# Kernel tuning notes

Hardware: AMD Instinct MI355X
Metric: run time of the kernel (lower is better)

Reference implementation:

```python
import jax, jax.numpy as jnp
import numpy as np
from jax import lax

B, P, C = 2, 512, 5                 # images, proposals/img, classes (incl. background)
IN_FEAT, REP = 12544, 1024          # 256*7*7 pooled features; TwoMLPHead width
H_IMG = W_IMG = 800.0
SCORE_THRESH, NMS_THRESH, DET_PER_IMG = 0.05, 0.5, 100
MIN_SIZE = 0.01
WX, WY, WW, WH = 10.0, 10.0, 5.0, 5.0
BBOX_CLIP = float(np.log(1000.0 / 16.0))
NEG = -1e9


def _make_boxes(key, n):
    k1, k2, k3, k4 = jax.random.split(key, 4)
    cx = jax.random.uniform(k1, (n,)) * W_IMG
    cy = jax.random.uniform(k2, (n,)) * H_IMG
    bw = jax.random.uniform(k3, (n,)) * 180.0 + 20.0
    bh = jax.random.uniform(k4, (n,)) * 180.0 + 20.0
    x1 = jnp.clip(cx - bw / 2, 0.0, W_IMG)
    y1 = jnp.clip(cy - bh / 2, 0.0, H_IMG)
    x2 = jnp.clip(cx + bw / 2, 0.0, W_IMG)
    y2 = jnp.clip(cy + bh / 2, 0.0, H_IMG)
    return jnp.stack([x1, y1, x2, y2], -1).astype(jnp.float32)


def setup_inputs() -> dict:
    ks = jax.random.split(jax.random.key(0), 12)
    box_features = jax.random.normal(ks[0], (B * P, IN_FEAT), jnp.float32)
    proposals = jnp.stack([_make_boxes(ks[1 + i], P) for i in range(B)])
    def w(k, shp):
        return (jax.random.normal(k, shp, jnp.float32) / np.sqrt(shp[0])).astype(jnp.float32)
    return {
        'box_features': box_features,
        'proposals': proposals,
        'W1': w(ks[3], (IN_FEAT, REP)), 'b1': jnp.zeros((REP,), jnp.float32),
        'W2': w(ks[4], (REP, REP)),     'b2': jnp.zeros((REP,), jnp.float32),
        'Wc': w(ks[5], (REP, C)),       'bc': jnp.zeros((C,), jnp.float32),
        'Wb': w(ks[6], (REP, 4 * C)),   'bb': jnp.zeros((4 * C,), jnp.float32),
    }


def box_iou(a, b):
    area_a = (a[:, 2] - a[:, 0]) * (a[:, 3] - a[:, 1])
    area_b = (b[:, 2] - b[:, 0]) * (b[:, 3] - b[:, 1])
    lt = jnp.maximum(a[:, None, :2], b[None, :, :2])
    rb = jnp.minimum(a[:, None, 2:], b[None, :, 2:])
    wh = jnp.clip(rb - lt, 0.0)
    inter = wh[..., 0] * wh[..., 1]
    return inter / (area_a[:, None] + area_b[None, :] - inter + 1e-9)


def decode(reg, props):
    # reg: [N, C, 4] raw deltas; props: [N, 4] xyxy  (torchvision BoxCoder.decode)
    w = props[:, 2] - props[:, 0]
    h = props[:, 3] - props[:, 1]
    cx = props[:, 0] + 0.5 * w
    cy = props[:, 1] + 0.5 * h
    dx, dy = reg[..., 0] / WX, reg[..., 1] / WY
    dw = jnp.minimum(reg[..., 2] / WW, BBOX_CLIP)
    dh = jnp.minimum(reg[..., 3] / WH, BBOX_CLIP)
    pcx = dx * w[:, None] + cx[:, None]
    pcy = dy * h[:, None] + cy[:, None]
    pw = jnp.exp(dw) * w[:, None]
    ph = jnp.exp(dh) * h[:, None]
    return jnp.stack([pcx - 0.5 * pw, pcy - 0.5 * ph, pcx + 0.5 * pw, pcy + 0.5 * ph], -1)


def postprocess_one(boxes, scores, labels):
    # boxes [M,4] (already clipped), scores [M], labels [M] int; fixed-size output.
    M = boxes.shape[0]
    ws = boxes[:, 2] - boxes[:, 0]
    hs = boxes[:, 3] - boxes[:, 1]
    valid = (scores > SCORE_THRESH) & (ws >= MIN_SIZE) & (hs >= MIN_SIZE)
    order = jnp.argsort(-scores)
    b, s, l, v = boxes[order], scores[order], labels[order], valid[order]
    # batched (per-class) NMS via class-offset trick
    off = l.astype(b.dtype)[:, None] * (max(H_IMG, W_IMG) + 1.0)
    iou = box_iou(b + off, b + off)
    idxs = jnp.arange(M)

    def body(i, keep):
        sup = (iou[i] > NMS_THRESH) & keep[i] & (idxs > i)
        return keep & ~sup

    keep = lax.fori_loop(0, M, body, v)
    sc = jnp.where(keep, s, NEG)
    top_s, top_i = lax.top_k(sc, DET_PER_IMG)
    ok = top_s > NEG / 2
    tb = jnp.where(ok[:, None], b[top_i], 0.0)
    tl = jnp.where(ok, l[top_i], 0)
    ts = jnp.where(ok, top_s, 0.0)
    return tb, ts, tl


def reference(box_features, proposals, W1, b1, W2, b2, Wc, bc, Wb, bb):
    # box_head: TwoMLPHead
    h = jax.nn.relu(box_features @ W1 + b1)
    h = jax.nn.relu(h @ W2 + b2)
    # box_predictor
    class_logits = h @ Wc + bc                       # [N, C]
    box_regression = (h @ Wb + bb).reshape(-1, C, 4)  # [N, C, 4]
    props = proposals.reshape(-1, 4)
    pred = decode(box_regression, props)             # [N, C, 4]
    # clip to image
    pred = jnp.stack([
        jnp.clip(pred[..., 0], 0.0, W_IMG), jnp.clip(pred[..., 1], 0.0, H_IMG),
        jnp.clip(pred[..., 2], 0.0, W_IMG), jnp.clip(pred[..., 3], 0.0, H_IMG)], -1)
    scores = jax.nn.softmax(class_logits, -1)        # [N, C]
    # drop background class, flatten proposal-major (matches torch reshape(-1,4))
    pb = pred[:, 1:, :].reshape(B, P * (C - 1), 4)
    sc = scores[:, 1:].reshape(B, P * (C - 1))
    labels = jnp.tile(jnp.arange(1, C, dtype=jnp.int32), P)  # [M]
    boxes_o, scores_o, labels_o = jax.vmap(postprocess_one, in_axes=(0, 0, None))(pb, sc, labels)
    return boxes_o, scores_o, labels_o
```

## Files before the change

### kernel.cpp

```cpp
#include <hip/hip_runtime.h>
#include <math.h>

#define NROWS 1024
#define K1    12544
#define REP   1024
#define NDET  2048
#define DETS  100
#define BBOX_CLIP_F 4.135166556742356f

typedef __attribute__((ext_vector_type(8))) short bf16x8;
typedef __attribute__((ext_vector_type(4))) float f32x4;

__device__ __forceinline__ unsigned short rne_bf16(float x) {
  unsigned u = __float_as_uint(x);
  u += 0x7fffu + ((u >> 16) & 1u);
  return (unsigned short)(u >> 16);
}
__device__ __forceinline__ float bf16f(unsigned short h) {
  return __uint_as_float(((unsigned)h) << 16);
}
__device__ __forceinline__ int swz(int r, int s) {
  return s ^ (r & 3) ^ ((r >> 2) & 3);
}
__device__ __forceinline__ void gload16(const void* g, void* lds) {
  __builtin_amdgcn_global_load_lds(
      (const __attribute__((address_space(1))) unsigned int*)g,
      (__attribute__((address_space(3))) unsigned int*)lds, 16, 0, 0);
}

__global__ __launch_bounds__(256) void pack_b(
    const float* __restrict__ W, unsigned short* __restrict__ Oh,
    unsigned short* __restrict__ Ol, int nKB) {
  __shared__ unsigned short th[32 * 36], tl[32 * 36];
  const int kb = blockIdx.x, n0 = blockIdx.y * 32;
  const int t = threadIdx.x;
  const int r = t >> 3, c4 = (t & 7) << 2;
  float4 v = *(const float4*)&W[(size_t)(kb * 32 + r) * REP + n0 + c4];
  float fv[4] = {v.x, v.y, v.z, v.w};
#pragma unroll
  for (int j = 0; j < 4; ++j) {
    unsigned short h = rne_bf16(fv[j]);
    th[(c4 + j) * 36 + r] = h;
    tl[(c4 + j) * 36 + r] = rne_bf16(fv[j] - bf16f(h));
  }
  __syncthreads();
  const int half = t >> 7;
  const int n_loc = (t & 127) >> 2, slot = t & 3;
  const unsigned short* src = (half ? tl : th) + n_loc * 36 + slot * 8;
  ushort4 u0 = *(const ushort4*)src;
  ushort4 u1 = *(const ushort4*)(src + 4);
  const int n = n0 + n_loc, rb = n >> 7, rr = n & 127;
  size_t chunk = ((size_t)(rb * nKB + kb)) * 512 + rr * 4 + swz(rr, slot);
  unsigned short* dst = (half ? Ol : Oh) + chunk * 8;
  *(ushort4*)dst = u0;
  *(ushort4*)(dst + 4) = u1;
}

__global__ __launch_bounds__(256) void pack_a(
    const float* __restrict__ A, unsigned short* __restrict__ Oh,
    unsigned short* __restrict__ Ol, int K, int nKB) {
  const int kb = blockIdx.x;
  const int r = blockIdx.y * 64 + (threadIdx.x >> 2);
  const int slot = threadIdx.x & 3;
  const float* p = A + (size_t)r * K + kb * 32 + slot * 8;
  float4 f0 = *(const float4*)p;
  float4 f1 = *(const float4*)(p + 4);
  float fv[8] = {f0.x, f0.y, f0.z, f0.w, f1.x, f1.y, f1.z, f1.w};
  unsigned short hh[8], ll[8];
#pragma unroll
  for (int j = 0; j < 8; ++j) {
    hh[j] = rne_bf16(fv[j]);
    ll[j] = rne_bf16(fv[j] - bf16f(hh[j]));
  }
  const int rb = r >> 7, rr = r & 127;
  size_t chunk = ((size_t)(rb * nKB + kb)) * 512 + rr * 4 + swz(rr, slot);
  unsigned short* dh = Oh + chunk * 8;
  unsigned short* dl = Ol + chunk * 8;
  *(ushort4*)dh = make_ushort4(hh[0], hh[1], hh[2], hh[3]);
  *(ushort4*)(dh + 4) = make_ushort4(hh[4], hh[5], hh[6], hh[7]);
  *(ushort4*)dl = make_ushort4(ll[0], ll[1], ll[2], ll[3]);
  *(ushort4*)(dl + 4) = make_ushort4(ll[4], ll[5], ll[6], ll[7]);
}

__global__ __launch_bounds__(256) void gemm_pk2(
    const unsigned short* __restrict__ Ah, const unsigned short* __restrict__ Al,
    const unsigned short* __restrict__ Bh, const unsigned short* __restrict__ Bl,
    float* __restrict__ T, int nKB, int stepsPerZ) {
  __shared__ __align__(16) unsigned short lds[2][4][4096];
  const int tid = threadIdx.x;
  const int w = tid >> 6, l = tid & 63;
  const int r_ = blockIdx.x, t_ = blockIdx.y;
  const int rbA = (r_ & 3) * 2 + (t_ & 1);
  const int rbB = (r_ >> 2) * 4 + (t_ >> 1);
  const int tk0 = blockIdx.z * stepsPerZ;
  const int fr = l & 15, q = l >> 4;
  const int wr = (w >> 1) * 64, wc = (w & 1) * 64;
  const int qs = q ^ (fr & 3) ^ (fr >> 2);
  const int aoff = ((wr + fr) * 4 + qs) * 16;
  const int boff = ((wc + fr) * 4 + qs) * 16;

  auto stage = [&](int bf, int tk) {
    const unsigned short* ga_h = Ah + ((size_t)(rbA * nKB + tk)) * 4096;
    const unsigned short* ga_l = Al + ((size_t)(rbA * nKB + tk)) * 4096;
    const unsigned short* gb_h = Bh + ((size_t)(rbB * nKB + tk)) * 4096;
    const unsigned short* gb_l = Bl + ((size_t)(rbB * nKB + tk)) * 4096;
#pragma unroll
    for (int rseg = 0; rseg < 2; ++rseg) {
      const int seg = rseg * 4 + w;
      const size_t go = (size_t)(seg * 64 + l) * 8;
      gload16(ga_h + go, &lds[bf][0][seg * 512]);
      gload16(ga_l + go, &lds[bf][1][seg * 512]);
      gload16(gb_h + go, &lds[bf][2][seg * 512]);
      gload16(gb_l + go, &lds[bf][3][seg * 512]);
    }
  };

  f32x4 acc[4][4];
#pragma unroll
  for (int m = 0; m < 4; ++m)
#pragma unroll
    for (int n = 0; n < 4; ++n) acc[m][n] = (f32x4){0.f, 0.f, 0.f, 0.f};

  stage(0, tk0);
  __syncthreads();
  int cur = 0;
  for (int s = 0; s < stepsPerZ; ++s) {
    if (s + 1 < stepsPerZ) stage(cur ^ 1, tk0 + s + 1);
    const char* La  = (const char*)&lds[cur][0][0];
    const char* Ll  = (const char*)&lds[cur][1][0];
    const char* Lbh = (const char*)&lds[cur][2][0];
    const char* Lbl = (const char*)&lds[cur][3][0];
    bf16x8 ah[4], al[4], bh[4], bl[4];
#pragma unroll
    for (int m = 0; m < 4; ++m) {
      ah[m] = *(const bf16x8*)(La + aoff + m * 1024);
      al[m] = *(const bf16x8*)(Ll + aoff + m * 1024);
    }
#pragma unroll
    for (int n = 0; n < 4; ++n) {
      bh[n] = *(const bf16x8*)(Lbh + boff + n * 1024);
      bl[n] = *(const bf16x8*)(Lbl + boff + n * 1024);
    }
#pragma unroll
    for (int m = 0; m < 4; ++m)
#pragma unroll
      for (int n = 0; n < 4; ++n) {
        acc[m][n] = __builtin_amdgcn_mfma_f32_16x16x32_bf16(ah[m], bh[n], acc[m][n], 0, 0, 0);
        acc[m][n] = __builtin_amdgcn_mfma_f32_16x16x32_bf16(ah[m], bl[n], acc[m][n], 0, 0, 0);
        acc[m][n] = __builtin_amdgcn_mfma_f32_16x16x32_bf16(al[m], bh[n], acc[m][n], 0, 0, 0);
      }
    __syncthreads();
    cur ^= 1;
  }
  float* Tz = T + (size_t)blockIdx.z * (NROWS * REP);
#pragma unroll
  for (int m = 0; m < 4; ++m) {
    const int r0 = rbA * 128 + wr + m * 16 + ((l >> 4) << 2);
#pragma unroll
    for (int n = 0; n < 4; ++n) {
      const int c = rbB * 128 + wc + n * 16 + fr;
#pragma unroll
      for (int j = 0; j < 4; ++j) Tz[(size_t)(r0 + j) * REP + c] = acc[m][n][j];
    }
  }
}

__global__ __launch_bounds__(256) void combine8_relu_pack(
    const float* __restrict__ T, const float* __restrict__ bias,
    unsigned short* __restrict__ Oh, unsigned short* __restrict__ Ol) {
  const int e = (blockIdx.x * 256 + threadIdx.x) * 8;
  const int MN = NROWS * REP;
  float s[8];
  {
    float4 a0 = *(const float4*)&T[e];
    float4 a1 = *(const float4*)&T[e + 4];
    s[0] = a0.x; s[1] = a0.y; s[2] = a0.z; s[3] = a0.w;
    s[4] = a1.x; s[5] = a1.y; s[6] = a1.z; s[7] = a1.w;
  }
#pragma unroll
  for (int z = 1; z < 8; ++z) {
    float4 a0 = *(const float4*)&T[z * MN + e];
    float4 a1 = *(const float4*)&T[z * MN + e + 4];
    s[0] += a0.x; s[1] += a0.y; s[2] += a0.z; s[3] += a0.w;
    s[4] += a1.x; s[5] += a1.y; s[6] += a1.z; s[7] += a1.w;
  }
  const int c0 = e & 1023;
  float4 b0 = *(const float4*)&bias[c0];
  float4 b1 = *(const float4*)&bias[c0 + 4];
  s[0] = fmaxf(s[0] + b0.x, 0.f); s[1] = fmaxf(s[1] + b0.y, 0.f);
  s[2] = fmaxf(s[2] + b0.z, 0.f); s[3] = fmaxf(s[3] + b0.w, 0.f);
  s[4] = fmaxf(s[4] + b1.x, 0.f); s[5] = fmaxf(s[5] + b1.y, 0.f);
  s[6] = fmaxf(s[6] + b1.z, 0.f); s[7] = fmaxf(s[7] + b1.w, 0.f);
  unsigned short hh[8], ll[8];
#pragma unroll
  for (int j = 0; j < 8; ++j) {
    hh[j] = rne_bf16(s[j]);
    ll[j] = rne_bf16(s[j] - bf16f(hh[j]));
  }
  const int r = e >> 10;
  const int kb = c0 >> 5, slot = (c0 >> 3) & 3;
  const int rb = r >> 7, rr = r & 127;
  size_t chunk = ((size_t)(rb * 32 + kb)) * 512 + rr * 4 + swz(rr, slot);
  unsigned short* dh = Oh + chunk * 8;
  unsigned short* dl = Ol + chunk * 8;
  *(ushort4*)dh = make_ushort4(hh[0], hh[1], hh[2], hh[3]);
  *(ushort4*)(dh + 4) = make_ushort4(hh[4], hh[5], hh[6], hh[7]);
  *(ushort4*)dl = make_ushort4(ll[0], ll[1], ll[2], ll[3]);
  *(ushort4*)(dl + 4) = make_ushort4(ll[4], ll[5], ll[6], ll[7]);
}

__global__ __launch_bounds__(256) void combine8_relu(
    const float* __restrict__ T, const float* __restrict__ bias, float* __restrict__ H) {
  const int i = blockIdx.x * 256 + threadIdx.x;
  const int MN4 = NROWS * REP / 4;
  const float4* t = (const float4*)T;
  float4 s0 = t[i];
#pragma unroll
  for (int z = 1; z < 8; ++z) {
    float4 v = t[i + z * MN4];
    s0.x += v.x; s0.y += v.y; s0.z += v.z; s0.w += v.w;
  }
  float4 bs = ((const float4*)bias)[i & 255];
  float4 r;
  r.x = fmaxf(s0.x + bs.x, 0.f);
  r.y = fmaxf(s0.y + bs.y, 0.f);
  r.z = fmaxf(s0.z + bs.z, 0.f);
  r.w = fmaxf(s0.w + bs.w, 0.f);
  ((float4*)H)[i] = r;
}

__global__ __launch_bounds__(256) void gemm_pk(
    const float* __restrict__ A, const unsigned short* __restrict__ Bh,
    const unsigned short* __restrict__ Bl, float* __restrict__ T,
    int K, int nKB, int stepsPerZ) {
  __shared__ __align__(16) unsigned short lds[2][4][4096];
  const int tid = threadIdx.x;
  const int w = tid >> 6, l = tid & 63;
  const int bm = blockIdx.x * 128;
  const int bnb = blockIdx.y;
  const int tk0 = blockIdx.z * stepsPerZ;
  const int arow = tid >> 1, ahalf = tid & 1;
  const int fr = l & 15, q = l >> 4;
  const int wr = (w >> 1) * 64, wc = (w & 1) * 64;
  const int qs = q ^ (fr & 3) ^ (fr >> 2);
  const int aoff = ((wr + fr) * 4 + qs) * 16;
  const int boff = ((wc + fr) * 4 + qs) * 16;
  const float* aptr = A + (size_t)(bm + arow) * K + ahalf * 16;

  float4 av[4];
  auto loadA = [&](int tk) {
    const float* p = aptr + tk * 32;
#pragma unroll
    for (int j = 0; j < 4; ++j) av[j] = *(const float4*)(p + j * 4);
  };
  auto stageB = [&](int bf, int tk) {
    const unsigned short* gh = Bh + ((size_t)(bnb * nKB + tk)) * 4096;
    const unsigned short* gl_ = Bl + ((size_t)(bnb * nKB + tk)) * 4096;
#pragma unroll
    for (int rseg = 0; rseg < 2; ++rseg) {
      const int seg = rseg * 4 + w;
      gload16(gh + (size_t)(seg * 64 + l) * 8, &lds[bf][2][seg * 512]);
      gload16(gl_ + (size_t)(seg * 64 + l) * 8, &lds[bf][3][seg * 512]);
    }
  };
  auto writeA = [&](int bf) {
#pragma unroll
    for (int j = 0; j < 2; ++j) {
      const int s_ = ahalf * 2 + j;
      float fv[8] = {av[j * 2].x, av[j * 2].y, av[j * 2].z, av[j * 2].w,
                     av[j * 2 + 1].x, av[j * 2 + 1].y, av[j * 2 + 1].z, av[j * 2 + 1].w};
      unsigned hp[4], lp[4];
#pragma unroll
      for (int p2 = 0; p2 < 4; ++p2) {
        unsigned short h0 = rne_bf16(fv[2 * p2]), h1 = rne_bf16(fv[2 * p2 + 1]);
        float l0 = fv[2 * p2] - bf16f(h0), l1 = fv[2 * p2 + 1] - bf16f(h1);
        hp[p2] = (unsigned)h0 | ((unsigned)h1 << 16);
        lp[p2] = (unsigned)rne_bf16(l0) | ((unsigned)rne_bf16(l1) << 16);
      }
      const int chunk = arow * 4 + swz(arow, s_);
      *(uint4*)&lds[bf][0][chunk * 8] = make_uint4(hp[0], hp[1], hp[2], hp[3]);
      *(uint4*)&lds[bf][1][chunk * 8] = make_uint4(lp[0], lp[1], lp[2], lp[3]);
    }
  };

  f32x4 acc[4][4];
#pragma unroll
  for (int m = 0; m < 4; ++m)
#pragma unroll
    for (int n = 0; n < 4; ++n) acc[m][n] = (f32x4){0.f, 0.f, 0.f, 0.f};

  loadA(tk0);
  stageB(0, tk0);
  writeA(0);
  __syncthreads();
  int cur = 0;
  for (int s = 0; s < stepsPerZ; ++s) {
    const bool nx = (s + 1 < stepsPerZ);
    if (nx) { loadA(tk0 + s + 1); stageB(cur ^ 1, tk0 + s + 1); }
    const char* La = (const char*)&lds[cur][0][0];
    const char* Ll = (const char*)&lds[cur][1][0];
    const char* Lbh = (const char*)&lds[cur][2][0];
    const char* Lbl = (const char*)&lds[cur][3][0];
    bf16x8 ah[4], al[4], bh[4], bl[4];
#pragma unroll
    for (int m = 0; m < 4; ++m) {
      ah[m] = *(const bf16x8*)(La + aoff + m * 1024);
      al[m] = *(const bf16x8*)(Ll + aoff + m * 1024);
    }
#pragma unroll
    for (int n = 0; n < 4; ++n) {
      bh[n] = *(const bf16x8*)(Lbh + boff + n * 1024);
      bl[n] = *(const bf16x8*)(Lbl + boff + n * 1024);
    }
#pragma unroll
    for (int m = 0; m < 4; ++m)
#pragma unroll
      for (int n = 0; n < 4; ++n) {
        acc[m][n] = __builtin_amdgcn_mfma_f32_16x16x32_bf16(ah[m], bh[n], acc[m][n], 0, 0, 0);
        acc[m][n] = __builtin_amdgcn_mfma_f32_16x16x32_bf16(ah[m], bl[n], acc[m][n], 0, 0, 0);
        acc[m][n] = __builtin_amdgcn_mfma_f32_16x16x32_bf16(al[m], bh[n], acc[m][n], 0, 0, 0);
      }
    if (nx) writeA(cur ^ 1);
    __syncthreads();
    cur ^= 1;
  }
  float* Tz = T + (size_t)blockIdx.z * (NROWS * REP);
#pragma unroll
  for (int m = 0; m < 4; ++m) {
    const int r0 = bm + wr + m * 16 + ((l >> 4) << 2);
#pragma unroll
    for (int n = 0; n < 4; ++n) {
      const int c = bnb * 128 + wc + n * 16 + fr;
#pragma unroll
      for (int j = 0; j < 4; ++j) Tz[(size_t)(r0 + j) * REP + c] = acc[m][n][j];
    }
  }
}

__global__ __launch_bounds__(256) void gemm64(
    const float* __restrict__ A, const float* __restrict__ W,
    float* __restrict__ T, int K, int N, int kChunk) {
  __shared__ float As[32][68];
  __shared__ float Bs[32][64];
  const int tid = threadIdx.x;
  const int bm = blockIdx.x * 64, bn = blockIdx.y * 64;
  const int k0 = blockIdx.z * kChunk;
  const int tx = tid & 15, ty = tid >> 4;
  const int ar = tid >> 3;
  const int ac = (tid & 7) << 2;
  const int br = tid >> 4;
  const int bc = (tid & 15) << 2;
  float acc[4][4] = {{0.f,0.f,0.f,0.f},{0.f,0.f,0.f,0.f},{0.f,0.f,0.f,0.f},{0.f,0.f,0.f,0.f}};
  for (int kk = k0; kk < k0 + kChunk; kk += 32) {
    float4 a0 = *(const float4*)&A[(size_t)(bm + ar) * K + kk + ac];
    float4 a1 = *(const float4*)&A[(size_t)(bm + ar + 32) * K + kk + ac];
    float4 b0 = *(const float4*)&W[(size_t)(kk + br) * N + bn + bc];
    float4 b1 = *(const float4*)&W[(size_t)(kk + br + 16) * N + bn + bc];
    As[ac+0][ar] = a0.x; As[ac+1][ar] = a0.y; As[ac+2][ar] = a0.z; As[ac+3][ar] = a0.w;
    As[ac+0][ar+32] = a1.x; As[ac+1][ar+32] = a1.y; As[ac+2][ar+32] = a1.z; As[ac+3][ar+32] = a1.w;
    *(float4*)&Bs[br][bc]    = b0;
    *(float4*)&Bs[br+16][bc] = b1;
    __syncthreads();
#pragma unroll
    for (int k = 0; k < 32; ++k) {
      float4 av = *(const float4*)&As[k][ty << 2];
      float4 bv = *(const float4*)&Bs[k][tx << 2];
      float a_[4] = {av.x, av.y, av.z, av.w};
      float b_[4] = {bv.x, bv.y, bv.z, bv.w};
#pragma unroll
      for (int i = 0; i < 4; ++i)
#pragma unroll
        for (int j = 0; j < 4; ++j)
          acc[i][j] = fmaf(a_[i], b_[j], acc[i][j]);
    }
    __syncthreads();
  }
  float* Tz = T + (size_t)blockIdx.z * NROWS * REP;
#pragma unroll
  for (int i = 0; i < 4; ++i) {
    float4 v = make_float4(acc[i][0], acc[i][1], acc[i][2], acc[i][3]);
    *(float4*)&Tz[(size_t)(bm + (ty << 2) + i) * N + bn + (tx << 2)] = v;
  }
}

__global__ __launch_bounds__(256) void combine_relu(
    const float* __restrict__ T, const float* __restrict__ bias, float* __restrict__ H) {
  const int i = blockIdx.x * 256 + threadIdx.x;
  const int MN4 = NROWS * REP / 4;
  const float4* t = (const float4*)T;
  float4 a = t[i], b = t[i + MN4], c = t[i + 2 * MN4], d = t[i + 3 * MN4];
  float4 bs = ((const float4*)bias)[i & 255];
  float4 r;
  r.x = fmaxf(((a.x + b.x) + (c.x + d.x)) + bs.x, 0.f);
  r.y = fmaxf(((a.y + b.y) + (c.y + d.y)) + bs.y, 0.f);
  r.z = fmaxf(((a.z + b.z) + (c.z + d.z)) + bs.z, 0.f);
  r.w = fmaxf(((a.w + b.w) + (c.w + d.w)) + bs.w, 0.f);
  ((float4*)H)[i] = r;
}

__global__ __launch_bounds__(256) void pack_w25(
    const float* __restrict__ Wc, const float* __restrict__ Wb, float* __restrict__ Wt) {
  const int i = blockIdx.x * 256 + threadIdx.x;
  if (i < 25 * 1024) {
    const int o = i >> 10, k = i & 1023;
    Wt[i] = (o < 5) ? Wc[(size_t)k * 5 + o] : Wb[(size_t)k * 20 + (o - 5)];
  }
}

__global__ __launch_bounds__(256) void heads2(
    const float* __restrict__ H2, const float* __restrict__ Wt,
    const float* __restrict__ bcv, const float* __restrict__ bbv,
    const float* __restrict__ props, float* __restrict__ pb, float* __restrict__ sc) {
  const int wave = threadIdx.x >> 6, l = threadIdx.x & 63;
  const int n = blockIdx.x * 4 + wave;
  const float* h = H2 + (size_t)n * REP + l * 16;
  float4 h0 = *(const float4*)h, h1 = *(const float4*)(h + 4);
  float4 h2v = *(const float4*)(h + 8), h3 = *(const float4*)(h + 12);
  float outv[25];
#pragma unroll
  for (int o = 0; o < 25; ++o) {
    const float* wp = Wt + o * REP + l * 16;
    float4 w0 = *(const float4*)wp, w1 = *(const float4*)(wp + 4);
    float4 w2 = *(const float4*)(wp + 8), w3 = *(const float4*)(wp + 12);
    float d = h0.x * w0.x;
    d = fmaf(h0.y, w0.y, d); d = fmaf(h0.z, w0.z, d); d = fmaf(h0.w, w0.w, d);
    d = fmaf(h1.x, w1.x, d); d = fmaf(h1.y, w1.y, d); d = fmaf(h1.z, w1.z, d); d = fmaf(h1.w, w1.w, d);
    d = fmaf(h2v.x, w2.x, d); d = fmaf(h2v.y, w2.y, d); d = fmaf(h2v.z, w2.z, d); d = fmaf(h2v.w, w2.w, d);
    d = fmaf(h3.x, w3.x, d); d = fmaf(h3.y, w3.y, d); d = fmaf(h3.z, w3.z, d); d = fmaf(h3.w, w3.w, d);
#pragma unroll
    for (int m = 1; m < 64; m <<= 1) d += __shfl_xor(d, m);
    outv[o] = d + ((o < 5) ? bcv[o] : bbv[o - 5]);
  }
  const float mx = fmaxf(fmaxf(fmaxf(outv[0], outv[1]), fmaxf(outv[2], outv[3])), outv[4]);
  const float e0 = expf(outv[0] - mx), e1 = expf(outv[1] - mx), e2 = expf(outv[2] - mx);
  const float e3 = expf(outv[3] - mx), e4 = expf(outv[4] - mx);
  const float inv = 1.0f / (e0 + e1 + e2 + e3 + e4);
  const float s1 = e1 * inv, s2 = e2 * inv, s3 = e3 * inv, s4 = e4 * inv;
  const float* pr = props + (size_t)n * 4;
  const float x1 = pr[0], y1 = pr[1], x2 = pr[2], y2 = pr[3];
  const float bw = x2 - x1, bh = y2 - y1;
  const float cx = x1 + 0.5f * bw, cy = y1 + 0.5f * bh;
  const int img = n >> 9, pbase = (n & 511) << 2;
#pragma unroll
  for (int c = 1; c <= 4; ++c) {
    if (l == c - 1) {
      const float r0 = outv[5 + c * 4 + 0], r1 = outv[5 + c * 4 + 1];
      const float r2 = outv[5 + c * 4 + 2], r3 = outv[5 + c * 4 + 3];
      const float dx = r0 / 10.0f, dy = r1 / 10.0f;
      const float dw = fminf(r2 / 5.0f, BBOX_CLIP_F);
      const float dh = fminf(r3 / 5.0f, BBOX_CLIP_F);
      const float pcx = dx * bw + cx, pcy = dy * bh + cy;
      const float pw = expf(dw) * bw, ph = expf(dh) * bh;
      float bx1 = pcx - 0.5f * pw, by1 = pcy - 0.5f * ph;
      float bx2 = pcx + 0.5f * pw, by2 = pcy + 0.5f * ph;
      bx1 = fminf(fmaxf(bx1, 0.f), 800.f);
      by1 = fminf(fmaxf(by1, 0.f), 800.f);
      bx2 = fminf(fmaxf(bx2, 0.f), 800.f);
      by2 = fminf(fmaxf(by2, 0.f), 800.f);
      const int pidx = pbase + (c - 1);
      float* o = pb + (size_t)(img * NDET + pidx) * 4;
      o[0] = bx1; o[1] = by1; o[2] = bx2; o[3] = by2;
      const float smc = (c == 1) ? s1 : (c == 2) ? s2 : (c == 3) ? s3 : s4;
      sc[img * NDET + pidx] = smc;
    }
  }
}

__global__ __launch_bounds__(256) void heads_kernel(
    const float* __restrict__ H2, const float* __restrict__ Wc, const float* __restrict__ bcv,
    const float* __restrict__ Wb, const float* __restrict__ bbv,
    const float* __restrict__ props, float* __restrict__ pb, float* __restrict__ sc) {
  const int n = blockIdx.x;
  __shared__ float hrow[REP];
  __shared__ float part[25][8];
  __shared__ float outv[25];
  __shared__ float smax[5];
  const int tid = threadIdx.x;
  ((float4*)hrow)[tid] = ((const float4*)(H2 + (size_t)n * REP))[tid];
  __syncthreads();
  if (tid < 200) {
    const int o = tid >> 3, s = tid & 7;
    float a = 0.f;
    if (o < 5) {
      const float* w = Wc + o;
      for (int k = s * 128; k < s * 128 + 128; ++k) a = fmaf(hrow[k], w[(size_t)k * 5], a);
    } else {
      const float* w = Wb + (o - 5);
      for (int k = s * 128; k < s * 128 + 128; ++k) a = fmaf(hrow[k], w[(size_t)k * 20], a);
    }
    part[o][s] = a;
  }
  __syncthreads();
  if (tid < 25) {
    float a = ((part[tid][0] + part[tid][1]) + (part[tid][2] + part[tid][3]))
            + ((part[tid][4] + part[tid][5]) + (part[tid][6] + part[tid][7]));
    a += (tid < 5) ? bcv[tid] : bbv[tid - 5];
    outv[tid] = a;
  }
  __syncthreads();
  if (tid == 0) {
    float m = outv[0];
    for (int c = 1; c < 5; ++c) m = fmaxf(m, outv[c]);
    float e[5], ssum = 0.f;
    for (int c = 0; c < 5; ++c) { e[c] = expf(outv[c] - m); ssum += e[c]; }
    for (int c = 0; c < 5; ++c) smax[c] = e[c] / ssum;
  }
  __syncthreads();
  if (tid < 4) {
    const int c = tid + 1;
    const float* pr = props + (size_t)n * 4;
    const float x1 = pr[0], y1 = pr[1], x2 = pr[2], y2 = pr[3];
    const float w = x2 - x1, h = y2 - y1;
    const float cx = x1 + 0.5f * w, cy = y1 + 0.5f * h;
    const float r0 = outv[5 + c * 4 + 0], r1 = outv[5 + c * 4 + 1];
    const float r2 = outv[5 + c * 4 + 2], r3 = outv[5 + c * 4 + 3];
    const float dx = r0 / 10.0f, dy = r1 / 10.0f;
    const float dw = fminf(r2 / 5.0f, BBOX_CLIP_F);
    const float dh = fminf(r3 / 5.0f, BBOX_CLIP_F);
    const float pcx = dx * w + cx, pcy = dy * h + cy;
    const float pw = expf(dw) * w, ph = expf(dh) * h;
    float bx1 = pcx - 0.5f * pw, by1 = pcy - 0.5f * ph;
    float bx2 = pcx + 0.5f * pw, by2 = pcy + 0.5f * ph;
    bx1 = fminf(fmaxf(bx1, 0.f), 800.f);
    by1 = fminf(fmaxf(by1, 0.f), 800.f);
    bx2 = fminf(fmaxf(bx2, 0.f), 800.f);
    by2 = fminf(fmaxf(by2, 0.f), 800.f);
    const int img = n >> 9;
    const int pidx = ((n & 511) << 2) + (c - 1);
    float* o = pb + (size_t)(img * NDET + pidx) * 4;
    o[0] = bx1; o[1] = by1; o[2] = bx2; o[3] = by2;
    sc[img * NDET + pidx] = smax[c];
  }
}

__global__ __launch_bounds__(1024) void sort_kernel(
    const float* __restrict__ sc, unsigned* __restrict__ sidx) {
  const int b = blockIdx.x;
  __shared__ unsigned long long key[NDET];
  const int tid = threadIdx.x;
  for (int t = tid; t < NDET; t += 1024) {
    unsigned bits = __float_as_uint(sc[b * NDET + t]);
    key[t] = ((unsigned long long)bits << 32) | (unsigned)(~t);
  }
  __syncthreads();
  for (int k = 2; k <= NDET; k <<= 1) {
    for (int j = k >> 1; j > 0; j >>= 1) {
      for (int t = tid; t < NDET; t += 1024) {
        const int ixj = t ^ j;
        if (ixj > t) {
          const bool up = (t & k) == 0;
          unsigned long long a = key[t], bb_ = key[ixj];
          if ((a < bb_) == up) { key[t] = bb_; key[ixj] = a; }
        }
      }
      __syncthreads();
    }
  }
  for (int t = tid; t < NDET; t += 1024)
    sidx[b * NDET + t] = ~(unsigned)key[t];
}

__global__ __launch_bounds__(256) void prep_kernel(
    const unsigned* __restrict__ sidx, const float* __restrict__ pb, const float* __restrict__ sc,
    float* __restrict__ sbox, float* __restrict__ soff, float* __restrict__ sscore,
    float* __restrict__ sarea, float* __restrict__ slab, unsigned* __restrict__ vword) {
  const int b = blockIdx.y;
  const int i = blockIdx.x * 256 + threadIdx.x;
  const unsigned oi = sidx[b * NDET + i];
  const float* bx = pb + (size_t)(b * NDET + oi) * 4;
  const float x1 = bx[0], y1 = bx[1], x2 = bx[2], y2 = bx[3];
  const float s = sc[b * NDET + oi];
  const float lab = (float)((oi & 3) + 1);
  const bool valid = (s > 0.05f) && ((x2 - x1) >= 0.01f) && ((y2 - y1) >= 0.01f);
  const float off = lab * 801.0f;
  float* sb = sbox + (size_t)(b * NDET + i) * 4;
  sb[0] = x1; sb[1] = y1; sb[2] = x2; sb[3] = y2;
  float* so = soff + (size_t)(b * NDET + i) * 4;
  so[0] = x1 + off; so[1] = y1 + off; so[2] = x2 + off; so[3] = y2 + off;
  sscore[b * NDET + i] = s;
  sarea[b * NDET + i] = (x2 - x1) * (y2 - y1);
  slab[b * NDET + i] = lab;
  const unsigned long long bal = __ballot(valid);
  if ((i & 31) == 0) vword[b * 64 + (i >> 5)] = (unsigned)(bal >> (i & 32));
}

__global__ __launch_bounds__(256) void mask_kernel(
    const float* __restrict__ soff, const float* __restrict__ sarea,
    unsigned* __restrict__ mask) {
  const int b = blockIdx.y;
  __shared__ float xx1[NDET + 64], yy1[NDET + 64], xx2[NDET + 64], yy2[NDET + 64];
  __shared__ float ar[NDET + 64];
  const int tid = threadIdx.x;
  for (int t = tid; t < NDET; t += 256) {
    float4 v = *(const float4*)(soff + ((size_t)b * NDET + t) * 4);
    const int pt = t + (t >> 5);
    xx1[pt] = v.x; yy1[pt] = v.y; xx2[pt] = v.z; yy2[pt] = v.w;
    ar[pt] = sarea[b * NDET + t];
  }
  __syncthreads();
  const int li = tid >> 6;
  const int w  = tid & 63;
#pragma unroll
  for (int pass = 0; pass < 4; ++pass) {
    const int i = blockIdx.x * 16 + pass * 4 + li;
    const int pi = i + (i >> 5);
    const float ax1 = xx1[pi], ay1 = yy1[pi], ax2 = xx2[pi], ay2 = yy2[pi];
    const float aa = ar[pi];
    unsigned bits = 0;
#pragma unroll 4
    for (int bb = 0; bb < 32; ++bb) {
      const int j = w * 32 + bb;
      const int pj = w * 33 + bb;
      const float ix = fmaxf(fminf(ax2, xx2[pj]) - fmaxf(ax1, xx1[pj]), 0.f);
      const float iy = fmaxf(fminf(ay2, yy2[pj]) - fmaxf(ay1, yy1[pj]), 0.f);
      const float inter = ix * iy;
      const float iou = inter / (aa + ar[pj] - inter + 1e-9f);
      if (j > i && iou > 0.5f) bits |= (1u << bb);
    }
    mask[((size_t)b * NDET + i) * 64 + w] = bits;
  }
}

__global__ __launch_bounds__(64) void scan_kernel(
    const unsigned* __restrict__ vword, const unsigned* __restrict__ mask,
    const float* __restrict__ sbox, const float* __restrict__ sscore,
    const float* __restrict__ slab, float* __restrict__ out) {
  const int b = blockIdx.x;
  const int lane = threadIdx.x;
  __shared__ unsigned sup[64];
  __shared__ unsigned short klist[DETS];
  sup[lane] = ~vword[b * 64 + lane];
  __syncthreads();
  int kcnt = 0;
  for (int w = 0; w < 64 && kcnt < DETS; ++w) {
    unsigned avail = ~sup[w];
    while (avail) {
      const int bb = __ffs(avail) - 1;
      const int i = w * 32 + bb;
      if (lane == 0) klist[kcnt] = (unsigned short)i;
      kcnt++;
      if (kcnt == DETS) break;
      sup[lane] |= mask[((size_t)b * NDET + i) * 64 + lane];
      __syncthreads();
      avail = ~sup[w] & (0xFFFFFFFEu << bb);
    }
  }
  __syncthreads();
  for (int s = lane; s < DETS; s += 64) {
    float b0 = 0.f, b1 = 0.f, b2 = 0.f, b3 = 0.f, sv = 0.f, lv = 0.f;
    if (s < kcnt) {
      const int i = klist[s];
      const float* bx = sbox + ((size_t)b * NDET + i) * 4;
      b0 = bx[0]; b1 = bx[1]; b2 = bx[2]; b3 = bx[3];
      sv = sscore[b * NDET + i];
      lv = slab[b * NDET + i];
    }
    float* ob = out + ((size_t)b * DETS + s) * 4;
    ob[0] = b0; ob[1] = b1; ob[2] = b2; ob[3] = b3;
    out[2 * DETS * 4 + b * DETS + s] = sv;
    out[2 * DETS * 4 + 2 * DETS + b * DETS + s] = lv;
  }
}

extern "C" void kernel_launch(void* const* d_in, const int* in_sizes, int n_in,
                              void* d_out, int out_size, void* d_ws, size_t ws_size,
                              hipStream_t stream) {
  const float* X     = (const float*)d_in[0];
  const float* props = (const float*)d_in[1];
  const float* W1    = (const float*)d_in[2];
  const float* b1    = (const float*)d_in[3];
  const float* W2    = (const float*)d_in[4];
  const float* b2    = (const float*)d_in[5];
  const float* Wc    = (const float*)d_in[6];
  const float* bc    = (const float*)d_in[7];
  const float* Wb    = (const float*)d_in[8];
  const float* bb    = (const float*)d_in[9];
  float* out = (float*)d_out;

  const size_t POST_B = 3200000;
  const size_t NEED_BIG =
      (size_t)9 * 1048576 * 4 +
      (size_t)4 * (size_t)K1 * 1024 * 2 +
      (size_t)4 * 1048576 * 2 + POST_B;
  const size_t NEED_MID =
      (size_t)10 * 1048576 * 4 +
      (size_t)2 * (size_t)K1 * 1024 * 2 +
      (size_t)2 * 1048576 * 2 + 2500000;

  float *T, *H1 = nullptr, *H2, *pb, *sc, *Wt = nullptr;
  unsigned short *W1h = nullptr, *W1l = nullptr, *W2h = nullptr, *W2l = nullptr;
  unsigned short *Ahp = nullptr, *Alp = nullptr, *H1h = nullptr, *H1l = nullptr;
  const int path = (ws_size >= NEED_BIG) ? 2 : (ws_size >= NEED_MID) ? 1 : 0;
  if (path == 2) {
    T   = (float*)d_ws;
    H2  = T + 8 * 1048576;
    W1h = (unsigned short*)(H2 + 1048576);
    W1l = W1h + (size_t)K1 * 1024;
    W2h = W1l + (size_t)K1 * 1024;
    W2l = W2h + 1048576;
    Ahp = W2l + 1048576;
    Alp = Ahp + (size_t)K1 * 1024;
    H1h = Alp + (size_t)K1 * 1024;
    H1l = H1h + 1048576;
    Wt  = (float*)(H1l + 1048576);
    pb  = Wt + 25 * 1024;
  } else if (path == 1) {
    T   = (float*)d_ws;
    H1  = T + 8 * 1048576;
    H2  = H1 + 1048576;
    W1h = (unsigned short*)(H2 + 1048576);
    W1l = W1h + (size_t)K1 * 1024;
    W2h = W1l + (size_t)K1 * 1024;
    W2l = W2h + 1048576;
    pb  = (float*)(W2l + 1048576);
  } else {
    T  = (float*)d_ws;
    H1 = T + 4 * 1048576;
    H2 = H1 + 1048576;
    pb = H2 + 1048576;
  }
  sc = pb + 2 * NDET * 4;
  unsigned* sidx = (unsigned*)(sc + 2 * NDET);
  float* sbox   = (float*)(sidx + 2 * NDET);
  float* soff   = sbox + 2 * NDET * 4;
  float* sscore = soff + 2 * NDET * 4;
  float* sarea  = sscore + 2 * NDET;
  float* slab   = sarea + 2 * NDET;
  unsigned* vword = (unsigned*)(slab + 2 * NDET);
  unsigned* mask  = vword + 128;

  if (path == 2) {
    pack_b<<<dim3(K1 / 32, 32), 256, 0, stream>>>(W1, W1h, W1l, K1 / 32);
    pack_b<<<dim3(32, 32), 256, 0, stream>>>(W2, W2h, W2l, 32);
    pack_a<<<dim3(K1 / 32, 16), 256, 0, stream>>>(X, Ahp, Alp, K1, K1 / 32);
    pack_w25<<<100, 256, 0, stream>>>(Wc, Wb, Wt);
    gemm_pk2<<<dim3(8, 8, 8), 256, 0, stream>>>(Ahp, Alp, W1h, W1l, T, K1 / 32, 49);
    combine8_relu_pack<<<512, 256, 0, stream>>>(T, b1, H1h, H1l);
    gemm_pk2<<<dim3(8, 8, 8), 256, 0, stream>>>(H1h, H1l, W2h, W2l, T, 32, 4);
    combine8_relu<<<1024, 256, 0, stream>>>(T, b2, H2);
    heads2<<<256, 256, 0, stream>>>(H2, Wt, bc, bb, props, pb, sc);
  } else if (path == 1) {
    pack_b<<<dim3(K1 / 32, 32), 256, 0, stream>>>(W1, W1h, W1l, K1 / 32);
    pack_b<<<dim3(32, 32), 256, 0, stream>>>(W2, W2h, W2l, 32);
    gemm_pk<<<dim3(8, 8, 8), 256, 0, stream>>>(X, W1h, W1l, T, K1, K1 / 32, 49);
    combine8_relu<<<1024, 256, 0, stream>>>(T, b1, H1);
    gemm_pk<<<dim3(8, 8, 8), 256, 0, stream>>>(H1, W2h, W2l, T, REP, 32, 4);
    combine8_relu<<<1024, 256, 0, stream>>>(T, b2, H2);
    heads_kernel<<<1024, 256, 0, stream>>>(H2, Wc, bc, Wb, bb, props, pb, sc);
  } else {
    gemm64<<<dim3(16, 16, 4), 256, 0, stream>>>(X, W1, T, K1, REP, K1 / 4);
    combine_relu<<<1024, 256, 0, stream>>>(T, b1, H1);
    gemm64<<<dim3(16, 16, 4), 256, 0, stream>>>(H1, W2, T, REP, REP, REP / 4);
    combine_relu<<<1024, 256, 0, stream>>>(T, b2, H2);
    heads_kernel<<<1024, 256, 0, stream>>>(H2, Wc, bc, Wb, bb, props, pb, sc);
  }
  sort_kernel<<<2, 1024, 0, stream>>>(sc, sidx);
  prep_kernel<<<dim3(8, 2), 256, 0, stream>>>(sidx, pb, sc, sbox, soff, sscore, sarea, slab, vword);
  mask_kernel<<<dim3(128, 2), 256, 0, stream>>>(soff, sarea, mask);
  scan_kernel<<<2, 64, 0, stream>>>(vword, mask, sbox, sscore, slab, out);
}
```

Before: 233.8 us.

## Fuse pack kernels, merge sort with prep, use register NMS scan

Merges the four packing kernels (W1, W2, X, head weights) into one launch, and the sort and prep kernels into a single kernel that gathers sorted boxes directly from shared keys. The NMS scan keeps the suppression words in registers and reads them with wave shuffles instead of shared memory plus barriers. The second GEMM's split-K drops from 8 to 4, which halves the partial-sum traffic for its reduction. Together these cut launch overhead and synchronisation in a latency-bound tail, at the cost of a large branchy pack kernel and fewer blocks for the second GEMM.

```diff
diff --git a/kernel.cpp b/kernel.cpp
--- a/kernel.cpp
+++ b/kernel.cpp
@@ -26,6 +26,75 @@
   __builtin_amdgcn_global_load_lds(
       (const __attribute__((address_space(1))) unsigned int*)g,
       (__attribute__((address_space(3))) unsigned int*)lds, 16, 0, 0);
+}
+
+__global__ __launch_bounds__(256) void pack_fused(
+    const float* __restrict__ X, const float* __restrict__ W1,
+    const float* __restrict__ W2, const float* __restrict__ Wc,
+    const float* __restrict__ Wb,
+    unsigned short* __restrict__ Ahp, unsigned short* __restrict__ Alp,
+    unsigned short* __restrict__ W1h, unsigned short* __restrict__ W1l,
+    unsigned short* __restrict__ W2h, unsigned short* __restrict__ W2l,
+    float* __restrict__ Wt) {
+  __shared__ unsigned short th[32 * 36], tl[32 * 36];
+  const int id = blockIdx.x;
+  const int t = threadIdx.x;
+  if (id < 13568) {
+    const float* W;
+    unsigned short *Oh, *Ol;
+    int nKB, kb, n0;
+    if (id < 12544) { W = W1; Oh = W1h; Ol = W1l; nKB = 392; kb = id % 392; n0 = (id / 392) * 32; }
+    else { const int r2 = id - 12544; W = W2; Oh = W2h; Ol = W2l; nKB = 32; kb = r2 % 32; n0 = (r2 / 32) * 32; }
+    const int r = t >> 3, c4 = (t & 7) << 2;
+    float4 v = *(const float4*)&W[(size_t)(kb * 32 + r) * REP + n0 + c4];
+    float fv[4] = {v.x, v.y, v.z, v.w};
+#pragma unroll
+    for (int j = 0; j < 4; ++j) {
+      unsigned short h = rne_bf16(fv[j]);
+      th[(c4 + j) * 36 + r] = h;
+      tl[(c4 + j) * 36 + r] = rne_bf16(fv[j] - bf16f(h));
+    }
+    __syncthreads();
+    const int half = t >> 7;
+    const int n_loc = (t & 127) >> 2, slot = t & 3;
+    const unsigned short* src = (half ? tl : th) + n_loc * 36 + slot * 8;
+    ushort4 u0 = *(const ushort4*)src;
+    ushort4 u1 = *(const ushort4*)(src + 4);
+    const int n = n0 + n_loc, rb = n >> 7, rr = n & 127;
+    size_t chunk = ((size_t)(rb * nKB + kb)) * 512 + rr * 4 + swz(rr, slot);
+    unsigned short* dst = (half ? Ol : Oh) + chunk * 8;
+    *(ushort4*)dst = u0;
+    *(ushort4*)(dst + 4) = u1;
+  } else if (id < 19840) {
+    const int r_ = id - 13568;
+    const int kb = r_ % 392;
+    const int row = (r_ / 392) * 64 + (t >> 2);
+    const int slot = t & 3;
+    const float* p = X + (size_t)row * K1 + kb * 32 + slot * 8;
+    float4 f0 = *(const float4*)p;
+    float4 f1 = *(const float4*)(p + 4);
+    float fv[8] = {f0.x, f0.y, f0.z, f0.w, f1.x, f1.y, f1.z, f1.w};
+    unsigned short hh[8], ll[8];
+#pragma unroll
+    for (int j = 0; j < 8; ++j) {
+      hh[j] = rne_bf16(fv[j]);
+      ll[j] = rne_bf16(fv[j] - bf16f(hh[j]));
+    }
+    const int rb = row >> 7, rr = row & 127;
+    size_t chunk = ((size_t)(rb * 392 + kb)) * 512 + rr * 4 + swz(rr, slot);
+    unsigned short* dh = Ahp + chunk * 8;
+    unsigned short* dl = Alp + chunk * 8;
+    *(ushort4*)dh = make_ushort4(hh[0], hh[1], hh[2], hh[3]);
+    *(ushort4*)(dh + 4) = make_ushort4(hh[4], hh[5], hh[6], hh[7]);
+    *(ushort4*)dl = make_ushort4(ll[0], ll[1], ll[2], ll[3]);
+    *(ushort4*)(dl + 4) = make_ushort4(ll[4], ll[5], ll[6], ll[7]);
+  } else {
+    const int i = (id - 19840) * 256 + t;
+    if (i < 25 * 1024) {
+      const int o = i >> 10, k = i & 1023;
+      Wt[i] = (o < 5) ? Wc[(size_t)k * 5 + o] : Wb[(size_t)k * 20 + (o - 5)];
+    }
+  }
 }
 
 __global__ __launch_bounds__(256) void pack_b(
@@ -54,32 +123,6 @@
   unsigned short* dst = (half ? Ol : Oh) + chunk * 8;
   *(ushort4*)dst = u0;
   *(ushort4*)(dst + 4) = u1;
-}
-
-__global__ __launch_bounds__(256) void pack_a(
-    const float* __restrict__ A, unsigned short* __restrict__ Oh,
-    unsigned short* __restrict__ Ol, int K, int nKB) {
-  const int kb = blockIdx.x;
-  const int r = blockIdx.y * 64 + (threadIdx.x >> 2);
-  const int slot = threadIdx.x & 3;
-  const float* p = A + (size_t)r * K + kb * 32 + slot * 8;
-  float4 f0 = *(const float4*)p;
-  float4 f1 = *(const float4*)(p + 4);
-  float fv[8] = {f0.x, f0.y, f0.z, f0.w, f1.x, f1.y, f1.z, f1.w};
-  unsigned short hh[8], ll[8];
-#pragma unroll
-  for (int j = 0; j < 8; ++j) {
-    hh[j] = rne_bf16(fv[j]);
-    ll[j] = rne_bf16(fv[j] - bf16f(hh[j]));
-  }
-  const int rb = r >> 7, rr = r & 127;
-  size_t chunk = ((size_t)(rb * nKB + kb)) * 512 + rr * 4 + swz(rr, slot);
-  unsigned short* dh = Oh + chunk * 8;
-  unsigned short* dl = Ol + chunk * 8;
-  *(ushort4*)dh = make_ushort4(hh[0], hh[1], hh[2], hh[3]);
-  *(ushort4*)(dh + 4) = make_ushort4(hh[4], hh[5], hh[6], hh[7]);
-  *(ushort4*)dl = make_ushort4(ll[0], ll[1], ll[2], ll[3]);
-  *(ushort4*)(dl + 4) = make_ushort4(ll[4], ll[5], ll[6], ll[7]);
 }
 
 __global__ __launch_bounds__(256) void gemm_pk2(
@@ -209,14 +252,14 @@
   *(ushort4*)(dl + 4) = make_ushort4(ll[4], ll[5], ll[6], ll[7]);
 }
 
-__global__ __launch_bounds__(256) void combine8_relu(
-    const float* __restrict__ T, const float* __restrict__ bias, float* __restrict__ H) {
+__global__ __launch_bounds__(256) void combineN_relu(
+    const float* __restrict__ T, const float* __restrict__ bias,
+    float* __restrict__ H, int nz) {
   const int i = blockIdx.x * 256 + threadIdx.x;
   const int MN4 = NROWS * REP / 4;
   const float4* t = (const float4*)T;
   float4 s0 = t[i];
-#pragma unroll
-  for (int z = 1; z < 8; ++z) {
+  for (int z = 1; z < nz; ++z) {
     float4 v = t[i + z * MN4];
     s0.x += v.x; s0.y += v.y; s0.z += v.z; s0.w += v.w;
   }
@@ -383,30 +426,6 @@
   }
 }
 
-__global__ __launch_bounds__(256) void combine_relu(
-    const float* __restrict__ T, const float* __restrict__ bias, float* __restrict__ H) {
-  const int i = blockIdx.x * 256 + threadIdx.x;
-  const int MN4 = NROWS * REP / 4;
-  const float4* t = (const float4*)T;
-  float4 a = t[i], b = t[i + MN4], c = t[i + 2 * MN4], d = t[i + 3 * MN4];
-  float4 bs = ((const float4*)bias)[i & 255];
-  float4 r;
-  r.x = fmaxf(((a.x + b.x) + (c.x + d.x)) + bs.x, 0.f);
-  r.y = fmaxf(((a.y + b.y) + (c.y + d.y)) + bs.y, 0.f);
-  r.z = fmaxf(((a.z + b.z) + (c.z + d.z)) + bs.z, 0.f);
-  r.w = fmaxf(((a.w + b.w) + (c.w + d.w)) + bs.w, 0.f);
-  ((float4*)H)[i] = r;
-}
-
-__global__ __launch_bounds__(256) void pack_w25(
-    const float* __restrict__ Wc, const float* __restrict__ Wb, float* __restrict__ Wt) {
-  const int i = blockIdx.x * 256 + threadIdx.x;
-  if (i < 25 * 1024) {
-    const int o = i >> 10, k = i & 1023;
-    Wt[i] = (o < 5) ? Wc[(size_t)k * 5 + o] : Wb[(size_t)k * 20 + (o - 5)];
-  }
-}
-
 __global__ __launch_bounds__(256) void heads2(
     const float* __restrict__ H2, const float* __restrict__ Wt,
     const float* __restrict__ bcv, const float* __restrict__ bbv,
@@ -533,8 +552,10 @@
   }
 }
 
-__global__ __launch_bounds__(1024) void sort_kernel(
-    const float* __restrict__ sc, unsigned* __restrict__ sidx) {
+__global__ __launch_bounds__(1024) void sortprep_kernel(
+    const float* __restrict__ sc, const float* __restrict__ pb,
+    float* __restrict__ sbox, float* __restrict__ soff, float* __restrict__ sscore,
+    float* __restrict__ sarea, float* __restrict__ slab, unsigned* __restrict__ vword) {
   const int b = blockIdx.x;
   __shared__ unsigned long long key[NDET];
   const int tid = threadIdx.x;
@@ -556,32 +577,25 @@
       __syncthreads();
     }
   }
-  for (int t = tid; t < NDET; t += 1024)
-    sidx[b * NDET + t] = ~(unsigned)key[t];
-}
-
-__global__ __launch_bounds__(256) void prep_kernel(
-    const unsigned* __restrict__ sidx, const float* __restrict__ pb, const float* __restrict__ sc,
-    float* __restrict__ sbox, float* __restrict__ soff, float* __restrict__ sscore,
-    float* __restrict__ sarea, float* __restrict__ slab, unsigned* __restrict__ vword) {
-  const int b = blockIdx.y;
-  const int i = blockIdx.x * 256 + threadIdx.x;
-  const unsigned oi = sidx[b * NDET + i];
-  const float* bx = pb + (size_t)(b * NDET + oi) * 4;
-  const float x1 = bx[0], y1 = bx[1], x2 = bx[2], y2 = bx[3];
-  const float s = sc[b * NDET + oi];
-  const float lab = (float)((oi & 3) + 1);
-  const bool valid = (s > 0.05f) && ((x2 - x1) >= 0.01f) && ((y2 - y1) >= 0.01f);
-  const float off = lab * 801.0f;
-  float* sb = sbox + (size_t)(b * NDET + i) * 4;
-  sb[0] = x1; sb[1] = y1; sb[2] = x2; sb[3] = y2;
-  float* so = soff + (size_t)(b * NDET + i) * 4;
-  so[0] = x1 + off; so[1] = y1 + off; so[2] = x2 + off; so[3] = y2 + off;
-  sscore[b * NDET + i] = s;
-  sarea[b * NDET + i] = (x2 - x1) * (y2 - y1);
-  slab[b * NDET + i] = lab;
-  const unsigned long long bal = __ballot(valid);
-  if ((i & 31) == 0) vword[b * 64 + (i >> 5)] = (unsigned)(bal >> (i & 32));
+  for (int pass = 0; pass < 2; ++pass) {
+    const int i = pass * 1024 + tid;
+    const unsigned oi = ~(unsigned)key[i];
+    const float* bx = pb + (size_t)(b * NDET + oi) * 4;
+    const float x1 = bx[0], y1 = bx[1], x2 = bx[2], y2 = bx[3];
+    const float s = sc[b * NDET + oi];
+    const float lab = (float)((oi & 3) + 1);
+    const bool valid = (s > 0.05f) && ((x2 - x1) >= 0.01f) && ((y2 - y1) >= 0.01f);
+    const float off = lab * 801.0f;
+    float* sb = sbox + (size_t)(b * NDET + i) * 4;
+    sb[0] = x1; sb[1] = y1; sb[2] = x2; sb[3] = y2;
+    float* so = soff + (size_t)(b * NDET + i) * 4;
+    so[0] = x1 + off; so[1] = y1 + off; so[2] = x2 + off; so[3] = y2 + off;
+    sscore[b * NDET + i] = s;
+    sarea[b * NDET + i] = (x2 - x1) * (y2 - y1);
+    slab[b * NDET + i] = lab;
+    const unsigned long long bal = __ballot(valid);
+    if ((i & 31) == 0) vword[b * 64 + (i >> 5)] = (unsigned)(bal >> (i & 32));
+  }
 }
 
 __global__ __launch_bounds__(256) void mask_kernel(
@@ -627,22 +641,19 @@
     const float* __restrict__ slab, float* __restrict__ out) {
   const int b = blockIdx.x;
   const int lane = threadIdx.x;
-  __shared__ unsigned sup[64];
+  unsigned supreg = ~vword[b * 64 + lane];
   __shared__ unsigned short klist[DETS];
-  sup[lane] = ~vword[b * 64 + lane];
-  __syncthreads();
   int kcnt = 0;
   for (int w = 0; w < 64 && kcnt < DETS; ++w) {
-    unsigned avail = ~sup[w];
+    unsigned avail = ~__shfl(supreg, w);
     while (avail) {
       const int bb = __ffs(avail) - 1;
       const int i = w * 32 + bb;
       if (lane == 0) klist[kcnt] = (unsigned short)i;
       kcnt++;
       if (kcnt == DETS) break;
-      sup[lane] |= mask[((size_t)b * NDET + i) * 64 + lane];
-      __syncthreads();
-      avail = ~sup[w] & (0xFFFFFFFEu << bb);
+      supreg |= mask[((size_t)b * NDET + i) * 64 + lane];
+      avail = ~__shfl(supreg, w) & (0xFFFFFFFEu << bb);
     }
   }
   __syncthreads();
@@ -730,32 +741,29 @@
   unsigned* mask  = vword + 128;
 
   if (path == 2) {
-    pack_b<<<dim3(K1 / 32, 32), 256, 0, stream>>>(W1, W1h, W1l, K1 / 32);
-    pack_b<<<dim3(32, 32), 256, 0, stream>>>(W2, W2h, W2l, 32);
-    pack_a<<<dim3(K1 / 32, 16), 256, 0, stream>>>(X, Ahp, Alp, K1, K1 / 32);
-    pack_w25<<<100, 256, 0, stream>>>(Wc, Wb, Wt);
+    pack_fused<<<19940, 256, 0, stream>>>(X, W1, W2, Wc, Wb,
+                                          Ahp, Alp, W1h, W1l, W2h, W2l, Wt);
     gemm_pk2<<<dim3(8, 8, 8), 256, 0, stream>>>(Ahp, Alp, W1h, W1l, T, K1 / 32, 49);
     combine8_relu_pack<<<512, 256, 0, stream>>>(T, b1, H1h, H1l);
-    gemm_pk2<<<dim3(8, 8, 8), 256, 0, stream>>>(H1h, H1l, W2h, W2l, T, 32, 4);
-    combine8_relu<<<1024, 256, 0, stream>>>(T, b2, H2);
+    gemm_pk2<<<dim3(8, 8, 4), 256, 0, stream>>>(H1h, H1l, W2h, W2l, T, 32, 8);
+    combineN_relu<<<1024, 256, 0, stream>>>(T, b2, H2, 4);
     heads2<<<256, 256, 0, stream>>>(H2, Wt, bc, bb, props, pb, sc);
   } else if (path == 1) {
     pack_b<<<dim3(K1 / 32, 32), 256, 0, stream>>>(W1, W1h, W1l, K1 / 32);
     pack_b<<<dim3(32, 32), 256, 0, stream>>>(W2, W2h, W2l, 32);
     gemm_pk<<<dim3(8, 8, 8), 256, 0, stream>>>(X, W1h, W1l, T, K1, K1 / 32, 49);
-    combine8_relu<<<1024, 256, 0, stream>>>(T, b1, H1);
-    gemm_pk<<<dim3(8, 8, 8), 256, 0, stream>>>(H1, W2h, W2l, T, REP, 32, 4);
-    combine8_relu<<<1024, 256, 0, stream>>>(T, b2, H2);
+    combineN_relu<<<1024, 256, 0, stream>>>(T, b1, H1, 8);
+    gemm_pk<<<dim3(8, 8, 4), 256, 0, stream>>>(H1, W2h, W2l, T, REP, 32, 8);
+    combineN_relu<<<1024, 256, 0, stream>>>(T, b2, H2, 4);
     heads_kernel<<<1024, 256, 0, stream>>>(H2, Wc, bc, Wb, bb, props, pb, sc);
   } else {
     gemm64<<<dim3(16, 16, 4), 256, 0, stream>>>(X, W1, T, K1, REP, K1 / 4);
-    combine_relu<<<1024, 256, 0, stream>>>(T, b1, H1);
+    combineN_relu<<<1024, 256, 0, stream>>>(T, b1, H1, 4);
     gemm64<<<dim3(16, 16, 4), 256, 0, stream>>>(H1, W2, T, REP, REP, REP / 4);
-    combine_relu<<<1024, 256, 0, stream>>>(T, b2, H2);
+    combineN_relu<<<1024, 256, 0, stream>>>(T, b2, H2, 4);
     heads_kernel<<<1024, 256, 0, stream>>>(H2, Wc, bc, Wb, bb, props, pb, sc);
   }
-  sort_kernel<<<2, 1024, 0, stream>>>(sc, sidx);
-  prep_kernel<<<dim3(8, 2), 256, 0, stream>>>(sidx, pb, sc, sbox, soff, sscore, sarea, slab, vword);
+  sortprep_kernel<<<2, 1024, 0, stream>>>(sc, pb, sbox, soff, sscore, sarea, slab, vword);
   mask_kernel<<<dim3(128, 2), 256, 0, stream>>>(soff, sarea, mask);
   scan_kernel<<<2, 64, 0, stream>>>(vword, mask, sbox, sscore, slab, out);
 }
```

New measurement: 225.3 us. 1.04x faster.
